# Kernel tuning notes

Measured on AMD Instinct MI355X. Metric: run time of the kernel, lower is better.

Reference implementation:

```python
import jax, jax.numpy as jnp
import numpy as np

T = 5          # Newton-Schulz iterations
EPS = 1e-05


def reference(X):
    # X: (B, C, L); training-mode IterNorm whitening with num_groups=1
    B, C, L = X.shape
    x = jnp.transpose(X, (1, 0, 2)).reshape(C, -1)        # (d, m)
    d, m = x.shape
    mean = jnp.mean(x, axis=-1, keepdims=True)
    xc = x - mean                                         # (d, m)
    I = jnp.eye(d, dtype=X.dtype)
    Sigma = I * EPS + (xc @ xc.T) * (1.0 / m)             # (d, d)
    rTr = 1.0 / jnp.trace(Sigma)                          # scalar
    Sigma_N = Sigma * rTr
    P = I
    for _ in range(T):
        P = 1.5 * P - 0.5 * (P @ P @ P) @ Sigma_N
    wm = P * jnp.sqrt(rTr)                                # whitening matrix
    xn = wm @ xc                                          # (d, m)
    Xn = jnp.transpose(xn.reshape(C, B, L), (1, 0, 2))
    return Xn


def setup_inputs() -> dict:
    key = jax.random.key(0)
    X = jax.random.normal(key, (32, 64, 8192), dtype=jnp.float32)
    return {"X": X}
```

## Files before the change

### kernel.cpp

```cpp
#include <hip/hip_runtime.h>
#include <math.h>

#define L_DIM   8192
#define NCH     64
#define M_TOT_F 262144.0f
#define EPS_F   1e-5f

typedef float f32x4 __attribute__((ext_vector_type(4)));
typedef short bf16x8 __attribute__((ext_vector_type(8)));

union U8 { unsigned u[4]; bf16x8 v; };

__device__ __forceinline__ void cvt2(float f0, float f1, unsigned& h, unsigned& l) {
    unsigned u0 = __float_as_uint(f0), u1 = __float_as_uint(f1);
    h = (u0 >> 16) | (u1 & 0xFFFF0000u);
    float r0 = f0 - __uint_as_float(u0 & 0xFFFF0000u);
    float r1 = f1 - __uint_as_float(u1 & 0xFFFF0000u);
    l = (__float_as_uint(r0) >> 16) | (__float_as_uint(r1) & 0xFFFF0000u);
}

__device__ __forceinline__ void split16(float v, unsigned short& h, unsigned short& l) {
    unsigned u = __float_as_uint(v);
    h = (unsigned short)(u >> 16);
    float r = v - __uint_as_float(u & 0xFFFF0000u);
    l = (unsigned short)(__float_as_uint(r) >> 16);
}

__device__ __forceinline__ f32x4 mfma16(bf16x8 a, bf16x8 b, f32x4 c) {
    return __builtin_amdgcn_mfma_f32_16x16x32_bf16(a, b, c, 0, 0, 0);
}

__device__ __forceinline__ f32x4 fzero() {
    f32x4 z; z[0] = 0.f; z[1] = 0.f; z[2] = 0.f; z[3] = 0.f; return z;
}

#define GTPB 4
__global__ __launch_bounds__(256) void gram_kernel(const float* __restrict__ X,
                                                   float* __restrict__ P) {
    __shared__ __align__(16) unsigned short hfrag[2][4096];
    __shared__ __align__(16) unsigned short lfrag[2][4096];
    const int tid  = threadIdx.x;
    const int w    = tid >> 6;
    const int lane = tid & 63;
    const int m    = lane & 15;
    const int q    = lane >> 4;
    const int row  = 16 * w + m;

    f32x4 acc1[4], acc2[4];
#pragma unroll
    for (int nb = 0; nb < 4; ++nb) { acc1[nb] = fzero(); acc2[nb] = fzero(); }
    float sacc = 0.f;

    const int tile0 = blockIdx.x * GTPB;
    float4 v[4];
    {
        int t = tile0;
        const float* src = X + ((size_t)((t >> 7) * NCH + row)) * L_DIM + ((t & 127) << 6) + 8 * q;
        v[0] = *(const float4*)(src);
        v[1] = *(const float4*)(src + 4);
        v[2] = *(const float4*)(src + 32);
        v[3] = *(const float4*)(src + 36);
    }

    for (int t = 0; t < GTPB; ++t) {
        const int p = t & 1;
#pragma unroll
        for (int i = 0; i < 4; ++i) sacc += v[i].x + v[i].y + v[i].z + v[i].w;

        bf16x8 Ah[2], Al[2];
#pragma unroll
        for (int k = 0; k < 2; ++k) {
            U8 H, L;
            cvt2(v[2 * k].x,     v[2 * k].y,     H.u[0], L.u[0]);
            cvt2(v[2 * k].z,     v[2 * k].w,     H.u[1], L.u[1]);
            cvt2(v[2 * k + 1].x, v[2 * k + 1].y, H.u[2], L.u[2]);
            cvt2(v[2 * k + 1].z, v[2 * k + 1].w, H.u[3], L.u[3]);
            Ah[k] = H.v; Al[k] = L.v;
            int chunk = ((w * 2 + k) * 4 + q) * 16 + m;
            *(bf16x8*)&hfrag[p][chunk * 8] = H.v;
            *(bf16x8*)&lfrag[p][chunk * 8] = L.v;
        }

        if (t + 1 < GTPB) {
            int tn = tile0 + t + 1;
            const float* src = X + ((size_t)((tn >> 7) * NCH + row)) * L_DIM + ((tn & 127) << 6) + 8 * q;
            v[0] = *(const float4*)(src);
            v[1] = *(const float4*)(src + 4);
            v[2] = *(const float4*)(src + 32);
            v[3] = *(const float4*)(src + 36);
        }
        __syncthreads();

#pragma unroll
        for (int k = 0; k < 2; ++k)
#pragma unroll
            for (int nb = 0; nb < 4; ++nb) {
                int chunk = ((nb * 2 + k) * 4 + q) * 16 + m;
                bf16x8 bh = *(const bf16x8*)&hfrag[p][chunk * 8];
                bf16x8 bl = *(const bf16x8*)&lfrag[p][chunk * 8];
                acc1[nb] = mfma16(Ah[k], bh, acc1[nb]);
                acc2[nb] = mfma16(Ah[k], bl, acc2[nb]);
            }
    }

    float* base = P + (size_t)blockIdx.x * 8256;
#pragma unroll
    for (int nb = 0; nb < 4; ++nb)
#pragma unroll
        for (int r = 0; r < 4; ++r) {
            int grow = 16 * w + 4 * q + r;
            int gcol = 16 * nb + m;
            base[grow * 64 + gcol]        = acc1[nb][r];
            base[4096 + grow * 64 + gcol] = acc2[nb][r];
        }
    sacc += __shfl_xor(sacc, 16);
    sacc += __shfl_xor(sacc, 32);
    if (q == 0) base[8192 + 16 * w + m] = sacc;
}

__global__ __launch_bounds__(256) void reduce_kernel(const float* __restrict__ P,
                                                     float* __restrict__ ws) {
    const int tid = threadIdx.x;
    const int w = tid >> 6, lane = tid & 63;
    const int e0 = blockIdx.x * 64;
    float a0 = 0.f, a1 = 0.f, a2 = 0.f, a3 = 0.f;
#pragma unroll 8
    for (int i = 0; i < 64; ++i) {
        const float* p = P + (size_t)(w * 256 + 4 * i) * 8256 + e0 + lane;
        a0 += p[0];
        a1 += p[8256];
        a2 += p[2 * 8256];
        a3 += p[3 * 8256];
    }
    float a = (a0 + a1) + (a2 + a3);
    __shared__ float red[4][64];
    red[w][lane] = a;
    __syncthreads();
    if (w == 0)
        ws[e0 + lane] = red[0][lane] + red[1][lane] + red[2][lane] + red[3][lane];
}

__device__ __forceinline__ void mm_core(f32x4* acc,
                                        const unsigned short* __restrict__ Xh,
                                        const unsigned short* __restrict__ Xl,
                                        const unsigned short* __restrict__ Yh,
                                        const unsigned short* __restrict__ Yl,
                                        int w, int m, int q) {
#pragma unroll
    for (int k0 = 0; k0 < 64; k0 += 32) {
        bf16x8 xh = *(const bf16x8*)&Xh[(16 * w + m) * 72 + k0 + 8 * q];
        bf16x8 xl = *(const bf16x8*)&Xl[(16 * w + m) * 72 + k0 + 8 * q];
#pragma unroll
        for (int nb = 0; nb < 4; ++nb) {
            bf16x8 yh = *(const bf16x8*)&Yh[(16 * nb + m) * 72 + k0 + 8 * q];
            bf16x8 yl = *(const bf16x8*)&Yl[(16 * nb + m) * 72 + k0 + 8 * q];
            acc[nb] = mfma16(xh, yh, acc[nb]);
            acc[nb] = mfma16(xh, yl, acc[nb]);
            acc[nb] = mfma16(xl, yh, acc[nb]);
        }
    }
}

__device__ __forceinline__ void mm_pl(unsigned short* __restrict__ Dh,
                                      unsigned short* __restrict__ Dl,
                                      const unsigned short* __restrict__ Xh,
                                      const unsigned short* __restrict__ Xl,
                                      const unsigned short* __restrict__ Yh,
                                      const unsigned short* __restrict__ Yl,
                                      int w, int m, int q) {
    f32x4 acc[4];
#pragma unroll
    for (int nb = 0; nb < 4; ++nb) acc[nb] = fzero();
    mm_core(acc, Xh, Xl, Yh, Yl, w, m, q);
#pragma unroll
    for (int nb = 0; nb < 4; ++nb)
#pragma unroll
        for (int r = 0; r < 4; ++r) {
            int row = 16 * w + 4 * q + r, col = 16 * nb + m;
            unsigned short h, l;
            split16(acc[nb][r], h, l);
            Dh[row * 72 + col] = h;
            Dl[row * 72 + col] = l;
        }
}

__global__ __launch_bounds__(256) void ns_kernel(float* __restrict__ ws) {
    __shared__ __align__(16) float Pf[64 * 68];
    __shared__ __align__(16) unsigned short Ph[64 * 72], Pl[64 * 72];
    __shared__ __align__(16) unsigned short Sh[64 * 72], Sl[64 * 72];
    __shared__ __align__(16) unsigned short T1h[64 * 72], T1l[64 * 72];
    __shared__ __align__(16) unsigned short T2h[64 * 72], T2l[64 * 72];
    __shared__ float mu[64];
    __shared__ float scal[2];

    const int tid = threadIdx.x;
    const int w = tid >> 6, lane = tid & 63;
    const int m = lane & 15, q = lane >> 4;
    const float inv_m = 1.0f / M_TOT_F;

    if (tid < 64) mu[tid] = ws[8192 + tid] * inv_m;
    __syncthreads();

    for (int e = tid; e < 4096; e += 256) {
        int i = e >> 6, j = e & 63;
        float g = (ws[e] + ws[4096 + e] + ws[4096 + (j << 6) + i]) * inv_m;
        Pf[i * 68 + j] = g - mu[i] * mu[j] + ((i == j) ? EPS_F : 0.f);
    }
    __syncthreads();

    if (tid < 64) {
        float v = Pf[tid * 68 + tid];
#pragma unroll
        for (int off = 32; off >= 1; off >>= 1) v += __shfl_xor(v, off);
        if (tid == 0) { scal[0] = 1.0f / v; scal[1] = sqrtf(1.0f / v); }
    }
    __syncthreads();
    const float rTr = scal[0];

    for (int e = tid; e < 4096; e += 256) {
        int i = e >> 6, j = e & 63;
        float sn = Pf[i * 68 + j] * rTr;
        unsigned short h, l;
        split16(sn, h, l);
        Sh[i * 72 + j] = h; Sl[i * 72 + j] = l;
        float pv = ((i == j) ? 1.5f : 0.f) - 0.5f * sn;
        Pf[i * 68 + j] = pv;
        split16(pv, h, l);
        Ph[i * 72 + j] = h; Pl[i * 72 + j] = l;
    }
    __syncthreads();

    for (int it = 0; it < 4; ++it) {
        mm_pl(T1h, T1l, Ph, Pl, Ph, Pl, w, m, q);
        __syncthreads();
        mm_pl(T2h, T2l, T1h, T1l, Ph, Pl, w, m, q);
        __syncthreads();
        f32x4 acc[4];
#pragma unroll
        for (int nb = 0; nb < 4; ++nb) acc[nb] = fzero();
        mm_core(acc, T2h, T2l, Sh, Sl, w, m, q);
#pragma unroll
        for (int nb = 0; nb < 4; ++nb)
#pragma unroll
            for (int r = 0; r < 4; ++r) {
                int row = 16 * w + 4 * q + r, col = 16 * nb + m;
                int idx = row * 68 + col;
                float pv = 1.5f * Pf[idx] - 0.5f * acc[nb][r];
                Pf[idx] = pv;
                unsigned short h, l;
                split16(pv, h, l);
                Ph[row * 72 + col] = h;
                Pl[row * 72 + col] = l;
            }
        __syncthreads();
    }

    const float s = scal[1];
    unsigned short* hp = (unsigned short*)ws;
    unsigned short* lp = hp + 4096;
    for (int e = tid; e < 4096; e += 256) {
        int i = e >> 6, j = e & 63;
        float v = Pf[i * 68 + j] * s;
        unsigned short h, l;
        split16(v, h, l);
        hp[e] = h;
        lp[e] = l;
    }
    if (tid < 64) {
        float a = 0.f;
#pragma unroll 8
        for (int k = 0; k < 64; ++k) a += Pf[tid * 68 + k] * mu[k];
        ws[8256 + tid] = -a * s;
    }
}

#define ATPB 4
__global__ __launch_bounds__(256) void apply_kernel(const float* __restrict__ X,
                                                    float* __restrict__ Y,
                                                    const float* __restrict__ ws) {
    __shared__ __align__(16) unsigned short hplane[2][4096];
    __shared__ __align__(16) unsigned short lplane[2][4096];
    const int tid  = threadIdx.x;
    const int w    = tid >> 6;
    const int lane = tid & 63;
    const int m    = lane & 15;
    const int q    = lane >> 4;
    const int cp   = tid & 31;
    const int lg   = tid >> 5;

    const unsigned short* hp = (const unsigned short*)ws;
    const unsigned short* lp = hp + 4096;
    bf16x8 Ah[2], Al[2];
#pragma unroll
    for (int kk = 0; kk < 2; ++kk) {
        Ah[kk] = *(const bf16x8*)&hp[(16 * w + m) * 64 + 32 * kk + 8 * q];
        Al[kk] = *(const bf16x8*)&lp[(16 * w + m) * 64 + 32 * kk + 8 * q];
    }
    const float4 bias4 = *(const float4*)&ws[8256 + 16 * w + 4 * q];

    float4 va[2], vb[2];
    {
        int tile = blockIdx.x * ATPB;
        const float* xb = X + (size_t)(tile >> 7) * (NCH * L_DIM) + ((tile & 127) << 6)
                          + (size_t)(2 * cp) * L_DIM + 4 * lg;
#pragma unroll
        for (int s = 0; s < 2; ++s) {
            va[s] = *(const float4*)(xb + 32 * s);
            vb[s] = *(const float4*)(xb + 32 * s + L_DIM);
        }
    }

    for (int t = 0; t < ATPB; ++t) {
        int tile = blockIdx.x * ATPB + t;
        int bidx = tile >> 7;
        int l0   = (tile & 127) << 6;
        const int p = t & 1;
        unsigned* hw = (unsigned*)hplane[p];
        unsigned* lw = (unsigned*)lplane[p];

#pragma unroll
        for (int s = 0; s < 2; ++s) {
            float fa[4], fb[4];
            *(float4*)fa = va[s];
            *(float4*)fb = vb[s];
#pragma unroll
            for (int i = 0; i < 4; ++i) {
                int l = 4 * lg + 32 * s + i;
                unsigned h, lo2;
                cvt2(fa[i], fb[i], h, lo2);
                int widx = l * 32 + (((cp >> 2) ^ (l & 7)) << 2) + (cp & 3);
                hw[widx] = h;
                lw[widx] = lo2;
            }
        }

        if (t + 1 < ATPB) {
            int tn = tile + 1;
            const float* xb = X + (size_t)(tn >> 7) * (NCH * L_DIM) + ((tn & 127) << 6)
                              + (size_t)(2 * cp) * L_DIM + 4 * lg;
#pragma unroll
            for (int s = 0; s < 2; ++s) {
                va[s] = *(const float4*)(xb + 32 * s);
                vb[s] = *(const float4*)(xb + 32 * s + L_DIM);
            }
        }
        __syncthreads();

        f32x4 acc[4];
#pragma unroll
        for (int nb = 0; nb < 4; ++nb) {
            acc[nb][0] = bias4.x; acc[nb][1] = bias4.y;
            acc[nb][2] = bias4.z; acc[nb][3] = bias4.w;
        }
#pragma unroll
        for (int kk = 0; kk < 2; ++kk)
#pragma unroll
            for (int nb = 0; nb < 4; ++nb) {
                int l = 16 * nb + m;
                int saddr = l * 64 + ((((4 * kk + q) ^ (l & 7))) << 3);
                bf16x8 bh = *(const bf16x8*)&hplane[p][saddr];
                bf16x8 bl = *(const bf16x8*)&lplane[p][saddr];
                acc[nb] = mfma16(Ah[kk], bh, acc[nb]);
                acc[nb] = mfma16(Ah[kk], bl, acc[nb]);
                acc[nb] = mfma16(Al[kk], bh, acc[nb]);
            }

#pragma unroll
        for (int nb = 0; nb < 4; ++nb)
#pragma unroll
            for (int rr = 0; rr < 4; ++rr)
                Y[((size_t)bidx * NCH + 16 * w + 4 * q + rr) * L_DIM + l0 + 16 * nb + m] = acc[nb][rr];
    }
}

extern "C" void kernel_launch(void* const* d_in, const int* in_sizes, int n_in,
                              void* d_out, int out_size, void* d_ws, size_t ws_size,
                              hipStream_t stream) {
    const float* X = (const float*)d_in[0];
    float* Y  = (float*)d_out;
    float* ws = (float*)d_ws;
    float* scratch = (float*)d_out;

    hipLaunchKernelGGL(gram_kernel,   dim3(1024), dim3(256), 0, stream, X, scratch);
    hipLaunchKernelGGL(reduce_kernel, dim3(129),  dim3(256), 0, stream, scratch, ws);
    hipLaunchKernelGGL(ns_kernel,     dim3(1),    dim3(256), 0, stream, ws);
    hipLaunchKernelGGL(apply_kernel,  dim3(1024), dim3(256), 0, stream, X, Y, ws);
}
```

Before: 157.2 us.

## Atomically reduce Gram partials and fuse Newton-Schulz into every apply block

Gram blocks now atomically add their partial sums into a zeroed workspace, which removes the separate reduce kernel and its scratch traffic. The single-block Newton-Schulz kernel is merged into the apply kernel, so each of 512 blocks recomputes the whitening matrix redundantly in shared memory before applying it. Tiles per block rise from 4 to 8 for both kernels. This cuts four launches down to two plus a memset and removes the serial one-block stage, at the cost of redundant per-block compute, atomic contention and nondeterministic float summation order.

```diff
diff --git a/kernel.cpp b/kernel.cpp
--- a/kernel.cpp
+++ b/kernel.cpp
@@ -5,6 +5,10 @@
 #define NCH     64
 #define M_TOT_F 262144.0f
 #define EPS_F   1e-5f
+#define GBLK    512
+#define GTPB    8
+#define ABLK    512
+#define ATPB    8
 
 typedef float f32x4 __attribute__((ext_vector_type(4)));
 typedef short bf16x8 __attribute__((ext_vector_type(8)));
@@ -26,6 +30,10 @@
     l = (unsigned short)(__float_as_uint(r) >> 16);
 }
 
+__device__ __forceinline__ float b2f(unsigned short h) {
+    return __uint_as_float(((unsigned)h) << 16);
+}
+
 __device__ __forceinline__ f32x4 mfma16(bf16x8 a, bf16x8 b, f32x4 c) {
     return __builtin_amdgcn_mfma_f32_16x16x32_bf16(a, b, c, 0, 0, 0);
 }
@@ -34,9 +42,8 @@
     f32x4 z; z[0] = 0.f; z[1] = 0.f; z[2] = 0.f; z[3] = 0.f; return z;
 }
 
-#define GTPB 4
 __global__ __launch_bounds__(256) void gram_kernel(const float* __restrict__ X,
-                                                   float* __restrict__ P) {
+                                                   float* __restrict__ ws) {
     __shared__ __align__(16) unsigned short hfrag[2][4096];
     __shared__ __align__(16) unsigned short lfrag[2][4096];
     const int tid  = threadIdx.x;
@@ -54,8 +61,8 @@
     const int tile0 = blockIdx.x * GTPB;
     float4 v[4];
     {
-        int t = tile0;
-        const float* src = X + ((size_t)((t >> 7) * NCH + row)) * L_DIM + ((t & 127) << 6) + 8 * q;
+        int t0 = tile0;
+        const float* src = X + ((size_t)((t0 >> 7) * NCH + row)) * L_DIM + ((t0 & 127) << 6) + 8 * q;
         v[0] = *(const float4*)(src);
         v[1] = *(const float4*)(src + 4);
         v[2] = *(const float4*)(src + 32);
@@ -103,48 +110,36 @@
             }
     }
 
-    float* base = P + (size_t)blockIdx.x * 8256;
 #pragma unroll
     for (int nb = 0; nb < 4; ++nb)
 #pragma unroll
         for (int r = 0; r < 4; ++r) {
             int grow = 16 * w + 4 * q + r;
             int gcol = 16 * nb + m;
-            base[grow * 64 + gcol]        = acc1[nb][r];
-            base[4096 + grow * 64 + gcol] = acc2[nb][r];
+            atomicAdd(&ws[grow * 64 + gcol],        acc1[nb][r]);
+            atomicAdd(&ws[4096 + grow * 64 + gcol], acc2[nb][r]);
         }
     sacc += __shfl_xor(sacc, 16);
     sacc += __shfl_xor(sacc, 32);
-    if (q == 0) base[8192 + 16 * w + m] = sacc;
-}
-
-__global__ __launch_bounds__(256) void reduce_kernel(const float* __restrict__ P,
-                                                     float* __restrict__ ws) {
-    const int tid = threadIdx.x;
-    const int w = tid >> 6, lane = tid & 63;
-    const int e0 = blockIdx.x * 64;
-    float a0 = 0.f, a1 = 0.f, a2 = 0.f, a3 = 0.f;
-#pragma unroll 8
-    for (int i = 0; i < 64; ++i) {
-        const float* p = P + (size_t)(w * 256 + 4 * i) * 8256 + e0 + lane;
-        a0 += p[0];
-        a1 += p[8256];
-        a2 += p[2 * 8256];
-        a3 += p[3 * 8256];
-    }
-    float a = (a0 + a1) + (a2 + a3);
-    __shared__ float red[4][64];
-    red[w][lane] = a;
-    __syncthreads();
-    if (w == 0)
-        ws[e0 + lane] = red[0][lane] + red[1][lane] + red[2][lane] + red[3][lane];
-}
+    if (q == 0) atomicAdd(&ws[8192 + row], sacc);
+}
+
+#define OFF_A      0
+#define OFF_T1H    0
+#define OFF_T1L    9216
+#define OFF_T2H    18432
+#define OFF_PH     32768
+#define OFF_PL     41984
+#define OFF_SH     51200
+#define OFF_SL     60416
+#define OFF_T2L    69632
+#define OFF_MU     78848
+#define OFF_SCAL   79104
+#define SM_BYTES   79120
 
 __device__ __forceinline__ void mm_core(f32x4* acc,
-                                        const unsigned short* __restrict__ Xh,
-                                        const unsigned short* __restrict__ Xl,
-                                        const unsigned short* __restrict__ Yh,
-                                        const unsigned short* __restrict__ Yl,
+                                        const unsigned short* Xh, const unsigned short* Xl,
+                                        const unsigned short* Yh, const unsigned short* Yl,
                                         int w, int m, int q) {
 #pragma unroll
     for (int k0 = 0; k0 < 64; k0 += 32) {
@@ -161,12 +156,9 @@
     }
 }
 
-__device__ __forceinline__ void mm_pl(unsigned short* __restrict__ Dh,
-                                      unsigned short* __restrict__ Dl,
-                                      const unsigned short* __restrict__ Xh,
-                                      const unsigned short* __restrict__ Xl,
-                                      const unsigned short* __restrict__ Yh,
-                                      const unsigned short* __restrict__ Yl,
+__device__ __forceinline__ void mm_pl(unsigned short* Dh, unsigned short* Dl,
+                                      const unsigned short* Xh, const unsigned short* Xl,
+                                      const unsigned short* Yh, const unsigned short* Yl,
                                       int w, int m, int q) {
     f32x4 acc[4];
 #pragma unroll
@@ -184,103 +176,12 @@
         }
 }
 
-__global__ __launch_bounds__(256) void ns_kernel(float* __restrict__ ws) {
-    __shared__ __align__(16) float Pf[64 * 68];
-    __shared__ __align__(16) unsigned short Ph[64 * 72], Pl[64 * 72];
-    __shared__ __align__(16) unsigned short Sh[64 * 72], Sl[64 * 72];
-    __shared__ __align__(16) unsigned short T1h[64 * 72], T1l[64 * 72];
-    __shared__ __align__(16) unsigned short T2h[64 * 72], T2l[64 * 72];
-    __shared__ float mu[64];
-    __shared__ float scal[2];
-
-    const int tid = threadIdx.x;
-    const int w = tid >> 6, lane = tid & 63;
-    const int m = lane & 15, q = lane >> 4;
-    const float inv_m = 1.0f / M_TOT_F;
-
-    if (tid < 64) mu[tid] = ws[8192 + tid] * inv_m;
-    __syncthreads();
-
-    for (int e = tid; e < 4096; e += 256) {
-        int i = e >> 6, j = e & 63;
-        float g = (ws[e] + ws[4096 + e] + ws[4096 + (j << 6) + i]) * inv_m;
-        Pf[i * 68 + j] = g - mu[i] * mu[j] + ((i == j) ? EPS_F : 0.f);
-    }
-    __syncthreads();
-
-    if (tid < 64) {
-        float v = Pf[tid * 68 + tid];
-#pragma unroll
-        for (int off = 32; off >= 1; off >>= 1) v += __shfl_xor(v, off);
-        if (tid == 0) { scal[0] = 1.0f / v; scal[1] = sqrtf(1.0f / v); }
-    }
-    __syncthreads();
-    const float rTr = scal[0];
-
-    for (int e = tid; e < 4096; e += 256) {
-        int i = e >> 6, j = e & 63;
-        float sn = Pf[i * 68 + j] * rTr;
-        unsigned short h, l;
-        split16(sn, h, l);
-        Sh[i * 72 + j] = h; Sl[i * 72 + j] = l;
-        float pv = ((i == j) ? 1.5f : 0.f) - 0.5f * sn;
-        Pf[i * 68 + j] = pv;
-        split16(pv, h, l);
-        Ph[i * 72 + j] = h; Pl[i * 72 + j] = l;
-    }
-    __syncthreads();
-
-    for (int it = 0; it < 4; ++it) {
-        mm_pl(T1h, T1l, Ph, Pl, Ph, Pl, w, m, q);
-        __syncthreads();
-        mm_pl(T2h, T2l, T1h, T1l, Ph, Pl, w, m, q);
-        __syncthreads();
-        f32x4 acc[4];
-#pragma unroll
-        for (int nb = 0; nb < 4; ++nb) acc[nb] = fzero();
-        mm_core(acc, T2h, T2l, Sh, Sl, w, m, q);
-#pragma unroll
-        for (int nb = 0; nb < 4; ++nb)
-#pragma unroll
-            for (int r = 0; r < 4; ++r) {
-                int row = 16 * w + 4 * q + r, col = 16 * nb + m;
-                int idx = row * 68 + col;
-                float pv = 1.5f * Pf[idx] - 0.5f * acc[nb][r];
-                Pf[idx] = pv;
-                unsigned short h, l;
-                split16(pv, h, l);
-                Ph[row * 72 + col] = h;
-                Pl[row * 72 + col] = l;
-            }
-        __syncthreads();
-    }
-
-    const float s = scal[1];
-    unsigned short* hp = (unsigned short*)ws;
-    unsigned short* lp = hp + 4096;
-    for (int e = tid; e < 4096; e += 256) {
-        int i = e >> 6, j = e & 63;
-        float v = Pf[i * 68 + j] * s;
-        unsigned short h, l;
-        split16(v, h, l);
-        hp[e] = h;
-        lp[e] = l;
-    }
-    if (tid < 64) {
-        float a = 0.f;
-#pragma unroll 8
-        for (int k = 0; k < 64; ++k) a += Pf[tid * 68 + k] * mu[k];
-        ws[8256 + tid] = -a * s;
-    }
-}
-
-#define ATPB 4
-__global__ __launch_bounds__(256) void apply_kernel(const float* __restrict__ X,
-                                                    float* __restrict__ Y,
-                                                    const float* __restrict__ ws) {
-    __shared__ __align__(16) unsigned short hplane[2][4096];
-    __shared__ __align__(16) unsigned short lplane[2][4096];
+__global__ __launch_bounds__(256, 2) void nsapply_kernel(const float* __restrict__ X,
+                                                         float* __restrict__ Y,
+                                                         const float* __restrict__ ws) {
+    __shared__ __align__(16) unsigned char smem[SM_BYTES];
     const int tid  = threadIdx.x;
+    const int bid  = blockIdx.x;
     const int w    = tid >> 6;
     const int lane = tid & 63;
     const int m    = lane & 15;
@@ -288,49 +189,134 @@
     const int cp   = tid & 31;
     const int lg   = tid >> 5;
 
-    const unsigned short* hp = (const unsigned short*)ws;
-    const unsigned short* lp = hp + 4096;
-    bf16x8 Ah[2], Al[2];
-#pragma unroll
-    for (int kk = 0; kk < 2; ++kk) {
-        Ah[kk] = *(const bf16x8*)&hp[(16 * w + m) * 64 + 32 * kk + 8 * q];
-        Al[kk] = *(const bf16x8*)&lp[(16 * w + m) * 64 + 32 * kk + 8 * q];
-    }
-    const float4 bias4 = *(const float4*)&ws[8256 + 16 * w + 4 * q];
+    unsigned short* hfrag = (unsigned short*)(smem + OFF_A);
+    unsigned short* lfrag = (unsigned short*)(smem + OFF_A + 16384);
+    unsigned short* Ph  = (unsigned short*)(smem + OFF_PH);
+    unsigned short* Pl  = (unsigned short*)(smem + OFF_PL);
+    unsigned short* Sh  = (unsigned short*)(smem + OFF_SH);
+    unsigned short* Sl  = (unsigned short*)(smem + OFF_SL);
+    unsigned short* T1h = (unsigned short*)(smem + OFF_T1H);
+    unsigned short* T1l = (unsigned short*)(smem + OFF_T1L);
+    unsigned short* T2h = (unsigned short*)(smem + OFF_T2H);
+    unsigned short* T2l = (unsigned short*)(smem + OFF_T2L);
+    float* mu   = (float*)(smem + OFF_MU);
+    float* scal = (float*)(smem + OFF_SCAL);
+    unsigned short* wmh = (unsigned short*)(smem + OFF_SH);
+    unsigned short* wml = (unsigned short*)(smem + OFF_SL);
+    float* bias = (float*)(smem + OFF_SH + 8192);
+    const float inv_m = 1.0f / M_TOT_F;
 
     float4 va[2], vb[2];
     {
-        int tile = blockIdx.x * ATPB;
+        int tile = bid * ATPB;
         const float* xb = X + (size_t)(tile >> 7) * (NCH * L_DIM) + ((tile & 127) << 6)
                           + (size_t)(2 * cp) * L_DIM + 4 * lg;
 #pragma unroll
-        for (int s = 0; s < 2; ++s) {
-            va[s] = *(const float4*)(xb + 32 * s);
-            vb[s] = *(const float4*)(xb + 32 * s + L_DIM);
-        }
-    }
+        for (int ss = 0; ss < 2; ++ss) {
+            va[ss] = *(const float4*)(xb + 32 * ss);
+            vb[ss] = *(const float4*)(xb + 32 * ss + L_DIM);
+        }
+    }
+
+    if (tid < 64) mu[tid] = ws[8192 + tid] * inv_m;
+    __syncthreads();
+
+    if (tid < 64) {
+        int e = tid * 65;
+        float g  = (ws[e] + 2.0f * ws[4096 + e]) * inv_m;
+        float sd = g - mu[tid] * mu[tid] + EPS_F;
+#pragma unroll
+        for (int off = 32; off >= 1; off >>= 1) sd += __shfl_xor(sd, off);
+        if (tid == 0) { scal[0] = 1.0f / sd; scal[1] = sqrtf(1.0f / sd); }
+    }
+    __syncthreads();
+    const float rTr = scal[0];
+
+    for (int e = tid; e < 4096; e += 256) {
+        int i = e >> 6, j = e & 63;
+        float g   = (ws[e] + ws[4096 + e] + ws[4096 + (j << 6) + i]) * inv_m;
+        float sig = g - mu[i] * mu[j] + ((i == j) ? EPS_F : 0.f);
+        float sn  = sig * rTr;
+        unsigned short h, l;
+        split16(sn, h, l);
+        Sh[i * 72 + j] = h; Sl[i * 72 + j] = l;
+        float pv = ((i == j) ? 1.5f : 0.f) - 0.5f * sn;
+        split16(pv, h, l);
+        Ph[i * 72 + j] = h; Pl[i * 72 + j] = l;
+    }
+    __syncthreads();
+
+    for (int it = 0; it < 4; ++it) {
+        mm_pl(T1h, T1l, Ph, Pl, Ph, Pl, w, m, q);
+        __syncthreads();
+        mm_pl(T2h, T2l, T1h, T1l, Ph, Pl, w, m, q);
+        __syncthreads();
+        f32x4 acc[4];
+#pragma unroll
+        for (int nb = 0; nb < 4; ++nb) acc[nb] = fzero();
+        mm_core(acc, T2h, T2l, Sh, Sl, w, m, q);
+#pragma unroll
+        for (int nb = 0; nb < 4; ++nb)
+#pragma unroll
+            for (int r = 0; r < 4; ++r) {
+                int row = 16 * w + 4 * q + r, col = 16 * nb + m;
+                int pidx = row * 72 + col;
+                float pold = b2f(Ph[pidx]) + b2f(Pl[pidx]);
+                float pv = 1.5f * pold - 0.5f * acc[nb][r];
+                unsigned short h, l;
+                split16(pv, h, l);
+                Ph[pidx] = h; Pl[pidx] = l;
+            }
+        __syncthreads();
+    }
+
+    const float s = scal[1];
+    if (tid < 64) {
+        float a = 0.f;
+#pragma unroll 8
+        for (int k = 0; k < 64; ++k)
+            a += (b2f(Ph[tid * 72 + k]) + b2f(Pl[tid * 72 + k])) * mu[k];
+        bias[tid] = -a * s;
+    }
+    for (int e = tid; e < 4096; e += 256) {
+        int i = e >> 6, j = e & 63;
+        float v = (b2f(Ph[i * 72 + j]) + b2f(Pl[i * 72 + j])) * s;
+        unsigned short h, l;
+        split16(v, h, l);
+        wmh[e] = h;
+        wml[e] = l;
+    }
+    __syncthreads();
+
+    bf16x8 Ah[2], Al[2];
+#pragma unroll
+    for (int kk = 0; kk < 2; ++kk) {
+        Ah[kk] = *(const bf16x8*)&wmh[(16 * w + m) * 64 + 32 * kk + 8 * q];
+        Al[kk] = *(const bf16x8*)&wml[(16 * w + m) * 64 + 32 * kk + 8 * q];
+    }
+    const float4 bias4 = *(const float4*)&bias[16 * w + 4 * q];
 
     for (int t = 0; t < ATPB; ++t) {
-        int tile = blockIdx.x * ATPB + t;
+        int tile = bid * ATPB + t;
         int bidx = tile >> 7;
         int l0   = (tile & 127) << 6;
         const int p = t & 1;
-        unsigned* hw = (unsigned*)hplane[p];
-        unsigned* lw = (unsigned*)lplane[p];
-
-#pragma unroll
-        for (int s = 0; s < 2; ++s) {
+        unsigned* hw2 = (unsigned*)(hfrag + p * 4096);
+        unsigned* lw2 = (unsigned*)(lfrag + p * 4096);
+
+#pragma unroll
+        for (int ss = 0; ss < 2; ++ss) {
             float fa[4], fb[4];
-            *(float4*)fa = va[s];
-            *(float4*)fb = vb[s];
+            *(float4*)fa = va[ss];
+            *(float4*)fb = vb[ss];
 #pragma unroll
             for (int i = 0; i < 4; ++i) {
-                int l = 4 * lg + 32 * s + i;
+                int l = 4 * lg + 32 * ss + i;
                 unsigned h, lo2;
                 cvt2(fa[i], fb[i], h, lo2);
                 int widx = l * 32 + (((cp >> 2) ^ (l & 7)) << 2) + (cp & 3);
-                hw[widx] = h;
-                lw[widx] = lo2;
+                hw2[widx] = h;
+                lw2[widx] = lo2;
             }
         }
 
@@ -339,9 +325,9 @@
             const float* xb = X + (size_t)(tn >> 7) * (NCH * L_DIM) + ((tn & 127) << 6)
                               + (size_t)(2 * cp) * L_DIM + 4 * lg;
 #pragma unroll
-            for (int s = 0; s < 2; ++s) {
-                va[s] = *(const float4*)(xb + 32 * s);
-                vb[s] = *(const float4*)(xb + 32 * s + L_DIM);
+            for (int ss = 0; ss < 2; ++ss) {
+                va[ss] = *(const float4*)(xb + 32 * ss);
+                vb[ss] = *(const float4*)(xb + 32 * ss + L_DIM);
             }
         }
         __syncthreads();
@@ -358,8 +344,8 @@
             for (int nb = 0; nb < 4; ++nb) {
                 int l = 16 * nb + m;
                 int saddr = l * 64 + ((((4 * kk + q) ^ (l & 7))) << 3);
-                bf16x8 bh = *(const bf16x8*)&hplane[p][saddr];
-                bf16x8 bl = *(const bf16x8*)&lplane[p][saddr];
+                bf16x8 bh = *(const bf16x8*)&hfrag[p * 4096 + saddr];
+                bf16x8 bl = *(const bf16x8*)&lfrag[p * 4096 + saddr];
                 acc[nb] = mfma16(Ah[kk], bh, acc[nb]);
                 acc[nb] = mfma16(Ah[kk], bl, acc[nb]);
                 acc[nb] = mfma16(Al[kk], bh, acc[nb]);
@@ -379,10 +365,8 @@
     const float* X = (const float*)d_in[0];
     float* Y  = (float*)d_out;
     float* ws = (float*)d_ws;
-    float* scratch = (float*)d_out;
-
-    hipLaunchKernelGGL(gram_kernel,   dim3(1024), dim3(256), 0, stream, X, scratch);
-    hipLaunchKernelGGL(reduce_kernel, dim3(129),  dim3(256), 0, stream, scratch, ws);
-    hipLaunchKernelGGL(ns_kernel,     dim3(1),    dim3(256), 0, stream, ws);
-    hipLaunchKernelGGL(apply_kernel,  dim3(1024), dim3(256), 0, stream, X, Y, ws);
-}
+
+    hipMemsetAsync(ws, 0, 8256 * sizeof(float), stream);
+    hipLaunchKernelGGL(gram_kernel,    dim3(GBLK), dim3(256), 0, stream, X, ws);
+    hipLaunchKernelGGL(nsapply_kernel, dim3(ABLK), dim3(256), 0, stream, X, Y, ws);
+}
```

New measurement: 163.8 us. 1.04x slower.

## Issue all tile loads upfront and split Newton-Schulz matmuls across eight waves

Applied to the files above, without the earlier changes.

The gram and apply kernels now issue global loads for all four tiles at the start instead of one tile ahead, so more memory requests are in flight per wave at the cost of more registers. The single-block Newton-Schulz kernel moves from 256 to 512 threads, with each wave computing a 16x32 output slice instead of 16x64. This halves the per-wave MFMA chain on the serial critical path. The trace is now computed directly from the diagonal, which removes one full-matrix pass and a barrier.

```diff
diff --git a/kernel.cpp b/kernel.cpp
--- a/kernel.cpp
+++ b/kernel.cpp
@@ -5,6 +5,8 @@
 #define NCH     64
 #define M_TOT_F 262144.0f
 #define EPS_F   1e-5f
+#define GTPB    4
+#define ATPB    4
 
 typedef float f32x4 __attribute__((ext_vector_type(4)));
 typedef short bf16x8 __attribute__((ext_vector_type(8)));
@@ -34,7 +36,6 @@
     f32x4 z; z[0] = 0.f; z[1] = 0.f; z[2] = 0.f; z[3] = 0.f; return z;
 }
 
-#define GTPB 4
 __global__ __launch_bounds__(256) void gram_kernel(const float* __restrict__ X,
                                                    float* __restrict__ P) {
     __shared__ __align__(16) unsigned short hfrag[2][4096];
@@ -52,42 +53,35 @@
     float sacc = 0.f;
 
     const int tile0 = blockIdx.x * GTPB;
-    float4 v[4];
-    {
-        int t = tile0;
-        const float* src = X + ((size_t)((t >> 7) * NCH + row)) * L_DIM + ((t & 127) << 6) + 8 * q;
-        v[0] = *(const float4*)(src);
-        v[1] = *(const float4*)(src + 4);
-        v[2] = *(const float4*)(src + 32);
-        v[3] = *(const float4*)(src + 36);
-    }
-
+    float4 v[GTPB][4];
+#pragma unroll
+    for (int t = 0; t < GTPB; ++t) {
+        int tt = tile0 + t;
+        const float* src = X + ((size_t)((tt >> 7) * NCH + row)) * L_DIM + ((tt & 127) << 6) + 8 * q;
+        v[t][0] = *(const float4*)(src);
+        v[t][1] = *(const float4*)(src + 4);
+        v[t][2] = *(const float4*)(src + 32);
+        v[t][3] = *(const float4*)(src + 36);
+    }
+
+#pragma unroll
     for (int t = 0; t < GTPB; ++t) {
         const int p = t & 1;
 #pragma unroll
-        for (int i = 0; i < 4; ++i) sacc += v[i].x + v[i].y + v[i].z + v[i].w;
+        for (int i = 0; i < 4; ++i) sacc += v[t][i].x + v[t][i].y + v[t][i].z + v[t][i].w;
 
         bf16x8 Ah[2], Al[2];
 #pragma unroll
         for (int k = 0; k < 2; ++k) {
             U8 H, L;
-            cvt2(v[2 * k].x,     v[2 * k].y,     H.u[0], L.u[0]);
-            cvt2(v[2 * k].z,     v[2 * k].w,     H.u[1], L.u[1]);
-            cvt2(v[2 * k + 1].x, v[2 * k + 1].y, H.u[2], L.u[2]);
-            cvt2(v[2 * k + 1].z, v[2 * k + 1].w, H.u[3], L.u[3]);
+            cvt2(v[t][2 * k].x,     v[t][2 * k].y,     H.u[0], L.u[0]);
+            cvt2(v[t][2 * k].z,     v[t][2 * k].w,     H.u[1], L.u[1]);
+            cvt2(v[t][2 * k + 1].x, v[t][2 * k + 1].y, H.u[2], L.u[2]);
+            cvt2(v[t][2 * k + 1].z, v[t][2 * k + 1].w, H.u[3], L.u[3]);
             Ah[k] = H.v; Al[k] = L.v;
             int chunk = ((w * 2 + k) * 4 + q) * 16 + m;
             *(bf16x8*)&hfrag[p][chunk * 8] = H.v;
             *(bf16x8*)&lfrag[p][chunk * 8] = L.v;
-        }
-
-        if (t + 1 < GTPB) {
-            int tn = tile0 + t + 1;
-            const float* src = X + ((size_t)((tn >> 7) * NCH + row)) * L_DIM + ((tn & 127) << 6) + 8 * q;
-            v[0] = *(const float4*)(src);
-            v[1] = *(const float4*)(src + 4);
-            v[2] = *(const float4*)(src + 32);
-            v[3] = *(const float4*)(src + 36);
         }
         __syncthreads();
 
@@ -115,7 +109,7 @@
         }
     sacc += __shfl_xor(sacc, 16);
     sacc += __shfl_xor(sacc, 32);
-    if (q == 0) base[8192 + 16 * w + m] = sacc;
+    if (q == 0) base[8192 + row] = sacc;
 }
 
 __global__ __launch_bounds__(256) void reduce_kernel(const float* __restrict__ P,
@@ -140,51 +134,46 @@
         ws[e0 + lane] = red[0][lane] + red[1][lane] + red[2][lane] + red[3][lane];
 }
 
-__device__ __forceinline__ void mm_core(f32x4* acc,
-                                        const unsigned short* __restrict__ Xh,
-                                        const unsigned short* __restrict__ Xl,
-                                        const unsigned short* __restrict__ Yh,
-                                        const unsigned short* __restrict__ Yl,
-                                        int w, int m, int q) {
+__device__ __forceinline__ void mm_core8(f32x4* acc,
+                                         const unsigned short* Xh, const unsigned short* Xl,
+                                         const unsigned short* Yh, const unsigned short* Yl,
+                                         int rg, int nbb, int m, int q) {
 #pragma unroll
     for (int k0 = 0; k0 < 64; k0 += 32) {
-        bf16x8 xh = *(const bf16x8*)&Xh[(16 * w + m) * 72 + k0 + 8 * q];
-        bf16x8 xl = *(const bf16x8*)&Xl[(16 * w + m) * 72 + k0 + 8 * q];
-#pragma unroll
-        for (int nb = 0; nb < 4; ++nb) {
+        bf16x8 xh = *(const bf16x8*)&Xh[(16 * rg + m) * 72 + k0 + 8 * q];
+        bf16x8 xl = *(const bf16x8*)&Xl[(16 * rg + m) * 72 + k0 + 8 * q];
+#pragma unroll
+        for (int j = 0; j < 2; ++j) {
+            int nb = nbb + j;
             bf16x8 yh = *(const bf16x8*)&Yh[(16 * nb + m) * 72 + k0 + 8 * q];
             bf16x8 yl = *(const bf16x8*)&Yl[(16 * nb + m) * 72 + k0 + 8 * q];
-            acc[nb] = mfma16(xh, yh, acc[nb]);
-            acc[nb] = mfma16(xh, yl, acc[nb]);
-            acc[nb] = mfma16(xl, yh, acc[nb]);
-        }
-    }
-}
-
-__device__ __forceinline__ void mm_pl(unsigned short* __restrict__ Dh,
-                                      unsigned short* __restrict__ Dl,
-                                      const unsigned short* __restrict__ Xh,
-                                      const unsigned short* __restrict__ Xl,
-                                      const unsigned short* __restrict__ Yh,
-                                      const unsigned short* __restrict__ Yl,
-                                      int w, int m, int q) {
-    f32x4 acc[4];
-#pragma unroll
-    for (int nb = 0; nb < 4; ++nb) acc[nb] = fzero();
-    mm_core(acc, Xh, Xl, Yh, Yl, w, m, q);
-#pragma unroll
-    for (int nb = 0; nb < 4; ++nb)
+            acc[j] = mfma16(xh, yh, acc[j]);
+            acc[j] = mfma16(xh, yl, acc[j]);
+            acc[j] = mfma16(xl, yh, acc[j]);
+        }
+    }
+}
+
+__device__ __forceinline__ void mm_pl8(unsigned short* Dh, unsigned short* Dl,
+                                       const unsigned short* Xh, const unsigned short* Xl,
+                                       const unsigned short* Yh, const unsigned short* Yl,
+                                       int rg, int nbb, int m, int q) {
+    f32x4 acc[2];
+    acc[0] = fzero(); acc[1] = fzero();
+    mm_core8(acc, Xh, Xl, Yh, Yl, rg, nbb, m, q);
+#pragma unroll
+    for (int j = 0; j < 2; ++j)
 #pragma unroll
         for (int r = 0; r < 4; ++r) {
-            int row = 16 * w + 4 * q + r, col = 16 * nb + m;
+            int row = 16 * rg + 4 * q + r, col = 16 * (nbb + j) + m;
             unsigned short h, l;
-            split16(acc[nb][r], h, l);
+            split16(acc[j][r], h, l);
             Dh[row * 72 + col] = h;
             Dl[row * 72 + col] = l;
         }
 }
 
-__global__ __launch_bounds__(256) void ns_kernel(float* __restrict__ ws) {
+__global__ __launch_bounds__(512) void ns_kernel(float* __restrict__ ws) {
     __shared__ __align__(16) float Pf[64 * 68];
     __shared__ __align__(16) unsigned short Ph[64 * 72], Pl[64 * 72];
     __shared__ __align__(16) unsigned short Sh[64 * 72], Sl[64 * 72];
@@ -194,32 +183,30 @@
     __shared__ float scal[2];
 
     const int tid = threadIdx.x;
-    const int w = tid >> 6, lane = tid & 63;
+    const int w8 = tid >> 6, lane = tid & 63;
     const int m = lane & 15, q = lane >> 4;
+    const int rg = w8 >> 1, nbb = (w8 & 1) << 1;
     const float inv_m = 1.0f / M_TOT_F;
 
     if (tid < 64) mu[tid] = ws[8192 + tid] * inv_m;
     __syncthreads();
 
-    for (int e = tid; e < 4096; e += 256) {
-        int i = e >> 6, j = e & 63;
-        float g = (ws[e] + ws[4096 + e] + ws[4096 + (j << 6) + i]) * inv_m;
-        Pf[i * 68 + j] = g - mu[i] * mu[j] + ((i == j) ? EPS_F : 0.f);
-    }
-    __syncthreads();
-
     if (tid < 64) {
-        float v = Pf[tid * 68 + tid];
-#pragma unroll
-        for (int off = 32; off >= 1; off >>= 1) v += __shfl_xor(v, off);
-        if (tid == 0) { scal[0] = 1.0f / v; scal[1] = sqrtf(1.0f / v); }
+        int e = tid * 65;
+        float g  = (ws[e] + 2.0f * ws[4096 + e]) * inv_m;
+        float sd = g - mu[tid] * mu[tid] + EPS_F;
+#pragma unroll
+        for (int off = 32; off >= 1; off >>= 1) sd += __shfl_xor(sd, off);
+        if (tid == 0) { scal[0] = 1.0f / sd; scal[1] = sqrtf(1.0f / sd); }
     }
     __syncthreads();
     const float rTr = scal[0];
 
-    for (int e = tid; e < 4096; e += 256) {
+    for (int e = tid; e < 4096; e += 512) {
         int i = e >> 6, j = e & 63;
-        float sn = Pf[i * 68 + j] * rTr;
+        float g   = (ws[e] + ws[4096 + e] + ws[4096 + (j << 6) + i]) * inv_m;
+        float sig = g - mu[i] * mu[j] + ((i == j) ? EPS_F : 0.f);
+        float sn  = sig * rTr;
         unsigned short h, l;
         split16(sn, h, l);
         Sh[i * 72 + j] = h; Sl[i * 72 + j] = l;
@@ -231,21 +218,20 @@
     __syncthreads();
 
     for (int it = 0; it < 4; ++it) {
-        mm_pl(T1h, T1l, Ph, Pl, Ph, Pl, w, m, q);
-        __syncthreads();
-        mm_pl(T2h, T2l, T1h, T1l, Ph, Pl, w, m, q);
-        __syncthreads();
-        f32x4 acc[4];
-#pragma unroll
-        for (int nb = 0; nb < 4; ++nb) acc[nb] = fzero();
-        mm_core(acc, T2h, T2l, Sh, Sl, w, m, q);
-#pragma unroll
-        for (int nb = 0; nb < 4; ++nb)
+        mm_pl8(T1h, T1l, Ph, Pl, Ph, Pl, rg, nbb, m, q);
+        __syncthreads();
+        mm_pl8(T2h, T2l, T1h, T1l, Ph, Pl, rg, nbb, m, q);
+        __syncthreads();
+        f32x4 acc[2];
+        acc[0] = fzero(); acc[1] = fzero();
+        mm_core8(acc, T2h, T2l, Sh, Sl, rg, nbb, m, q);
+#pragma unroll
+        for (int j = 0; j < 2; ++j)
 #pragma unroll
             for (int r = 0; r < 4; ++r) {
-                int row = 16 * w + 4 * q + r, col = 16 * nb + m;
+                int row = 16 * rg + 4 * q + r, col = 16 * (nbb + j) + m;
                 int idx = row * 68 + col;
-                float pv = 1.5f * Pf[idx] - 0.5f * acc[nb][r];
+                float pv = 1.5f * Pf[idx] - 0.5f * acc[j][r];
                 Pf[idx] = pv;
                 unsigned short h, l;
                 split16(pv, h, l);
@@ -258,7 +244,7 @@
     const float s = scal[1];
     unsigned short* hp = (unsigned short*)ws;
     unsigned short* lp = hp + 4096;
-    for (int e = tid; e < 4096; e += 256) {
+    for (int e = tid; e < 4096; e += 512) {
         int i = e >> 6, j = e & 63;
         float v = Pf[i * 68 + j] * s;
         unsigned short h, l;
@@ -274,7 +260,6 @@
     }
 }
 
-#define ATPB 4
 __global__ __launch_bounds__(256) void apply_kernel(const float* __restrict__ X,
                                                     float* __restrict__ Y,
                                                     const float* __restrict__ ws) {
@@ -298,50 +283,41 @@
     }
     const float4 bias4 = *(const float4*)&ws[8256 + 16 * w + 4 * q];
 
-    float4 va[2], vb[2];
-    {
-        int tile = blockIdx.x * ATPB;
+    float4 va[ATPB][2], vb[ATPB][2];
+#pragma unroll
+    for (int t = 0; t < ATPB; ++t) {
+        int tile = blockIdx.x * ATPB + t;
         const float* xb = X + (size_t)(tile >> 7) * (NCH * L_DIM) + ((tile & 127) << 6)
                           + (size_t)(2 * cp) * L_DIM + 4 * lg;
 #pragma unroll
-        for (int s = 0; s < 2; ++s) {
-            va[s] = *(const float4*)(xb + 32 * s);
-            vb[s] = *(const float4*)(xb + 32 * s + L_DIM);
-        }
-    }
-
+        for (int ss = 0; ss < 2; ++ss) {
+            va[t][ss] = *(const float4*)(xb + 32 * ss);
+            vb[t][ss] = *(const float4*)(xb + 32 * ss + L_DIM);
+        }
+    }
+
+#pragma unroll
     for (int t = 0; t < ATPB; ++t) {
         int tile = blockIdx.x * ATPB + t;
         int bidx = tile >> 7;
         int l0   = (tile & 127) << 6;
         const int p = t & 1;
-        unsigned* hw = (unsigned*)hplane[p];
-        unsigned* lw = (unsigned*)lplane[p];
-
-#pragma unroll
-        for (int s = 0; s < 2; ++s) {
+        unsigned* hw2 = (unsigned*)hplane[p];
+        unsigned* lw2 = (unsigned*)lplane[p];
+
+#pragma unroll
+        for (int ss = 0; ss < 2; ++ss) {
             float fa[4], fb[4];
-            *(float4*)fa = va[s];
-            *(float4*)fb = vb[s];
+            *(float4*)fa = va[t][ss];
+            *(float4*)fb = vb[t][ss];
 #pragma unroll
             for (int i = 0; i < 4; ++i) {
-                int l = 4 * lg + 32 * s + i;
+                int l = 4 * lg + 32 * ss + i;
                 unsigned h, lo2;
                 cvt2(fa[i], fb[i], h, lo2);
                 int widx = l * 32 + (((cp >> 2) ^ (l & 7)) << 2) + (cp & 3);
-                hw[widx] = h;
-                lw[widx] = lo2;
-            }
-        }
-
-        if (t + 1 < ATPB) {
-            int tn = tile + 1;
-            const float* xb = X + (size_t)(tn >> 7) * (NCH * L_DIM) + ((tn & 127) << 6)
-                              + (size_t)(2 * cp) * L_DIM + 4 * lg;
-#pragma unroll
-            for (int s = 0; s < 2; ++s) {
-                va[s] = *(const float4*)(xb + 32 * s);
-                vb[s] = *(const float4*)(xb + 32 * s + L_DIM);
+                hw2[widx] = h;
+                lw2[widx] = lo2;
             }
         }
         __syncthreads();
@@ -383,6 +359,6 @@
 
     hipLaunchKernelGGL(gram_kernel,   dim3(1024), dim3(256), 0, stream, X, scratch);
     hipLaunchKernelGGL(reduce_kernel, dim3(129),  dim3(256), 0, stream, scratch, ws);
-    hipLaunchKernelGGL(ns_kernel,     dim3(1),    dim3(256), 0, stream, ws);
+    hipLaunchKernelGGL(ns_kernel,     dim3(1),    dim3(512), 0, stream, ws);
     hipLaunchKernelGGL(apply_kernel,  dim3(1024), dim3(256), 0, stream, X, Y, ws);
 }
```

Result: faster. 153.8 us (-2.2%).
